# Kernel optimization log

Measured on AMD Instinct MI355X. Metric: run time of the kernel, lower is better.

Reference implementation:

```python
import jax, jax.numpy as jnp
import numpy as np

B, C, H, W = 2, 3, 96, 96
D = 32  # qkv channels

def setup_inputs() -> dict:
    key = jax.random.key(0)
    ks = jax.random.split(key, 9)
    s3 = 1.0 / np.sqrt(3.0)
    sD = 1.0 / np.sqrt(float(D))
    return {
        "image": jax.random.normal(ks[0], (B, C, H, W), dtype=jnp.float32),
        "key_w": jax.random.normal(ks[1], (D, C), dtype=jnp.float32) * s3,
        "key_b": jax.random.normal(ks[2], (D,), dtype=jnp.float32) * 0.01,
        "query_w": jax.random.normal(ks[3], (D, C), dtype=jnp.float32) * s3,
        "query_b": jax.random.normal(ks[4], (D,), dtype=jnp.float32) * 0.01,
        "value_w": jax.random.normal(ks[5], (D, C), dtype=jnp.float32) * s3,
        "value_b": jax.random.normal(ks[6], (D,), dtype=jnp.float32) * 0.01,
        "out_w": jax.random.normal(ks[7], (C, D), dtype=jnp.float32) * sD,
        "out_b": jax.random.normal(ks[8], (C,), dtype=jnp.float32) * 0.01,
    }

def reference(image, key_w, key_b, query_w, query_b, value_w, value_b, out_w, out_b):
    b, c, h, w = image.shape
    n = h * w
    x = image.reshape(b, c, n)  # [B,3,N]
    # 1x1 convs == per-pixel linear maps over channels
    f_x = jnp.einsum('dc,bcn->bdn', key_w, x) + key_b[None, :, None]    # key   [B,D,N]
    g_x = jnp.einsum('dc,bcn->bdn', query_w, x) + query_b[None, :, None]  # query [B,D,N]
    h_x = jnp.einsum('dc,bcn->bdn', value_w, x) + value_b[None, :, None]  # value [B,D,N]
    # s = f_x^T @ g_x : [B,N,N]; softmax over dim=1 (first N axis), as in torch code
    s = jnp.einsum('bdn,bdm->bnm', f_x, g_x)
    beta = jax.nn.softmax(s, axis=1)
    # v = h_x @ beta : [B,D,N]
    v = jnp.einsum('bdn,bnm->bdm', h_x, beta)
    # output 1x1 conv D->3, then clamp
    o = jnp.einsum('cd,bdm->bcm', out_w, v) + out_b[None, :, None]
    o = jnp.clip(o, -1.0, 1.0)
    return o.reshape(b, c, h, w)
```

## Files before the change

kernel.cpp:

```cpp
#include <hip/hip_runtime.h>
#include <hip/hip_fp16.h>

#define BB 2
#define CC 3
#define NN 9216
#define DD 32
#define NSPLIT 4
#define KSPLIT 6
#define KEYS_PER_WAVE (NN / (KSPLIT * NSPLIT))
#define CHUNKS (KEYS_PER_WAVE / 64)
#define NGROUP (BB * NN / 32)
#define L2E 1.44269504f
#define SZH ((size_t)BB * NN * DD)

typedef _Float16 half8 __attribute__((ext_vector_type(8)));
typedef _Float16 half4v __attribute__((ext_vector_type(4)));
typedef __fp16 fp16x2 __attribute__((ext_vector_type(2)));
typedef float float4v __attribute__((ext_vector_type(4)));

#define MFMA_K32(a, b, c) __builtin_amdgcn_mfma_f32_16x16x32_f16((a), (b), (c), 0, 0, 0)

__global__ __launch_bounds__(256) void prep_kernel(
    const float* __restrict__ img,
    const float* __restrict__ kw, const float* __restrict__ kb,
    const float* __restrict__ qw, const float* __restrict__ qb,
    const float* __restrict__ vw, const float* __restrict__ vb,
    const float* __restrict__ ow,
    _Float16* __restrict__ fH, _Float16* __restrict__ fL,
    _Float16* __restrict__ gH, _Float16* __restrict__ gL,
    _Float16* __restrict__ hP)
{
    __shared__ float wsm[256];
    __shared__ float cwb[12];
    int bid = blockIdx.x;
    int t = threadIdx.x;
    if (bid < 288) {
        float v;
        if (t < 96)       v = kw[t];
        else if (t < 192) v = qw[t - 96];
        else if (t < 224) v = kb[t - 192];
        else              v = qb[t - 224];
        wsm[t] = v;
        __syncthreads();

        int id = bid * 256 + t;
        int part = id & 3;
        int n = (id >> 2) % NN;
        int b = (id >> 2) / NN;
        const float* xb = img + (size_t)b * CC * NN + n;
        float x0 = xb[0], x1 = xb[NN], x2 = xb[2 * NN];
        half8 fh, fl, gh, gl;
#pragma unroll
        for (int j = 0; j < 8; j++) {
            int d = part * 8 + j;
            float fv = wsm[d * 3 + 0] * x0 + wsm[d * 3 + 1] * x1 +
                       wsm[d * 3 + 2] * x2 + wsm[192 + d];
            float gv = (wsm[96 + d * 3 + 0] * x0 + wsm[96 + d * 3 + 1] * x1 +
                        wsm[96 + d * 3 + 2] * x2 + wsm[224 + d]) * L2E;
            _Float16 fhi = (_Float16)fv;
            _Float16 ghi = (_Float16)gv;
            fh[j] = fhi; fl[j] = (_Float16)(fv - (float)fhi);
            gh[j] = ghi; gl[j] = (_Float16)(gv - (float)ghi);
        }
        size_t off = ((size_t)b * NN + n) * DD + part * 8;
        *(half8*)(fH + off) = fh;
        *(half8*)(fL + off) = fl;
        *(half8*)(gH + off) = gh;
        *(half8*)(gL + off) = gl;
    } else {
        if (t < 9) {
            int c = t / 3, k = t % 3;
            float s = 0.f;
#pragma unroll
            for (int d = 0; d < DD; d++) s += ow[c * DD + d] * vw[d * 3 + k];
            cwb[t] = s;
        } else if (t < 12) {
            int c = t - 9;
            float s = 0.f;
#pragma unroll
            for (int d = 0; d < DD; d++) s += ow[c * DD + d] * vb[d];
            cwb[9 + c] = s;
        }
        __syncthreads();
        const int N8 = NN / 8;
        int id = (bid - 288) * 256 + t;
        int n8 = id % N8;
        int row = (id / N8) & 3;
        int b = id / (N8 * 4);
        half8 hv = {1, 1, 1, 1, 1, 1, 1, 1};
        if (row < 3) {
            const float* xb = img + (size_t)b * CC * NN + n8 * 8;
            float w0 = cwb[row * 3 + 0], w1 = cwb[row * 3 + 1],
                  w2 = cwb[row * 3 + 2], bv = cwb[9 + row];
#pragma unroll
            for (int j = 0; j < 8; j++)
                hv[j] = (_Float16)(w0 * xb[j] + w1 * xb[NN + j] + w2 * xb[2 * NN + j] + bv);
        }
        *(half8*)(hP + ((size_t)(b * 4 + row)) * NN + n8 * 8) = hv;
    }
}

__device__ __forceinline__ void softmax_store(const float4v* s, float& mrun,
                                              float4v& acc, _Float16* Pw,
                                              int l16, int quad)
{
    float a0 = fmaxf(fmaxf(s[0][0], s[0][1]), s[0][2]);
    float a1 = fmaxf(fmaxf(s[0][3], s[1][0]), s[1][1]);
    float a2 = fmaxf(fmaxf(s[1][2], s[1][3]), s[2][0]);
    float a3 = fmaxf(fmaxf(s[2][1], s[2][2]), s[2][3]);
    float a4 = fmaxf(fmaxf(s[3][0], s[3][1]), s[3][2]);
    float lmax = fmaxf(fmaxf(fmaxf(a0, a1), fmaxf(a2, a3)), fmaxf(a4, s[3][3]));
    if (__any(lmax > mrun + 8.f)) {
        float mx = fmaxf(lmax, __shfl_xor(lmax, 16, 64));
        mx = fmaxf(mx, __shfl_xor(mx, 32, 64));
        float mnew = fmaxf(mrun, mx);
        float alpha = __builtin_amdgcn_exp2f(mrun - mnew);
#pragma unroll
        for (int r = 0; r < 4; r++) acc[r] *= alpha;
        mrun = mnew;
    }
#pragma unroll
    for (int blk = 0; blk < 4; blk++) {
        float p0 = __builtin_amdgcn_exp2f(s[blk][0] - mrun);
        float p1 = __builtin_amdgcn_exp2f(s[blk][1] - mrun);
        float p2 = __builtin_amdgcn_exp2f(s[blk][2] - mrun);
        float p3 = __builtin_amdgcn_exp2f(s[blk][3] - mrun);
        union { fp16x2 h2[2]; half4v h4; } u;
        u.h2[0] = __builtin_amdgcn_cvt_pkrtz(p0, p1);
        u.h2[1] = __builtin_amdgcn_cvt_pkrtz(p2, p3);
        *(half4v*)(Pw + l16 * 72 + blk * 16 + quad * 4) = u.h4;
    }
}

__global__ __launch_bounds__(256)
__attribute__((amdgpu_waves_per_eu(4, 4)))
void attn_partial_kernel(
    const _Float16* __restrict__ ws,
    float* __restrict__ pnum, float* __restrict__ pM)
{
    const _Float16* fH = ws;
    const _Float16* gH = ws + 2 * SZH;
    const _Float16* hP = ws + 4 * SZH;

    const int gb = blockIdx.x;
    const int g  = gb / KSPLIT;
    const int ks = gb % KSPLIT;
    const int b = g / (NN / 32);
    const int m0 = (g % (NN / 32)) * 32;
    const int tid = threadIdx.x;
    const int w = tid >> 6;
    const int lane = tid & 63;
    const int l16 = lane & 15;
    const int quad = lane >> 4;

    union SMem {
        _Float16 P[NSPLIT * 2 * 16 * 72];
        struct { float acc[NSPLIT][4][33]; float mbuf[NSPLIT][32]; } mg;
    };
    __shared__ __align__(16) SMem sm;

    const _Float16* gHb = gH + ((size_t)b * NN + m0 + l16) * DD + quad * 8;
    half8 qh0 = *(const half8*)(gHb);
    half8 ql0 = *(const half8*)(gHb + SZH);
    half8 qh1 = *(const half8*)(gHb + (size_t)16 * DD);
    half8 ql1 = *(const half8*)(gHb + SZH + (size_t)16 * DD);

    float4v acc0 = {0,0,0,0};
    float4v acc1 = {0,0,0,0};
    float mrun0 = -1e30f;
    float mrun1 = -1e30f;

    const int nbase = ks * (NN / KSPLIT) + w * KEYS_PER_WAVE;
    const int vrow = (l16 < 3) ? l16 : 3;
    const _Float16* vp = hP + ((size_t)(b * 4 + vrow)) * NN + nbase + quad * 8;
    const _Float16* kp = fH + ((size_t)b * NN + nbase + l16) * DD + quad * 8;
    const _Float16* lp = kp + SZH;
    _Float16* Pw0 = sm.P + (size_t)(w * 2 + 0) * 16 * 72;
    _Float16* Pw1 = sm.P + (size_t)(w * 2 + 1) * 16 * 72;

    half8 kC[4], lC[4];
#pragma unroll
    for (int blk = 0; blk < 4; blk++) {
        kC[blk] = *(const half8*)(kp + (size_t)(blk * 16) * DD);
        lC[blk] = *(const half8*)(lp + (size_t)(blk * 16) * DD);
    }
    kp += (size_t)64 * DD;
    lp += (size_t)64 * DD;

    for (int c = 0; c < CHUNKS; ++c) {
        float4v s[4];
#pragma unroll
        for (int blk = 0; blk < 4; blk++) {
            float4v z = {0,0,0,0};
            float4v t0 = MFMA_K32(kC[blk], ql0, z);
            t0 = MFMA_K32(lC[blk], qh0, t0);
            s[blk] = MFMA_K32(kC[blk], qh0, t0);
        }
        softmax_store(s, mrun0, acc0, Pw0, l16, quad);

#pragma unroll
        for (int blk = 0; blk < 4; blk++) {
            float4v z = {0,0,0,0};
            float4v t1 = MFMA_K32(kC[blk], ql1, z);
            t1 = MFMA_K32(lC[blk], qh1, t1);
            s[blk] = MFMA_K32(kC[blk], qh1, t1);
            kC[blk] = *(const half8*)(kp + (size_t)(blk * 16) * DD);
            lC[blk] = *(const half8*)(lp + (size_t)(blk * 16) * DD);
        }
        kp += (size_t)64 * DD;
        lp += (size_t)64 * DD;

        half8 vA0 = *(const half8*)(vp);
        half8 vA1 = *(const half8*)(vp + 32);

        softmax_store(s, mrun1, acc1, Pw1, l16, quad);

        {
            half8 pf0 = *(const half8*)(Pw0 + l16 * 72 + quad * 8);
            half8 pf1 = *(const half8*)(Pw0 + l16 * 72 + 32 + quad * 8);
            acc0 = MFMA_K32(vA0, pf0, acc0);
            acc0 = MFMA_K32(vA1, pf1, acc0);
            half8 qf0 = *(const half8*)(Pw1 + l16 * 72 + quad * 8);
            half8 qf1 = *(const half8*)(Pw1 + l16 * 72 + 32 + quad * 8);
            acc1 = MFMA_K32(vA0, qf0, acc1);
            acc1 = MFMA_K32(vA1, qf1, acc1);
        }
        vp += 64;
    }

    __syncthreads();

    if (quad == 0) {
#pragma unroll
        for (int r = 0; r < 4; r++) {
            sm.mg.acc[w][r][l16]      = acc0[r];
            sm.mg.acc[w][r][l16 + 16] = acc1[r];
        }
        sm.mg.mbuf[w][l16]      = mrun0;
        sm.mg.mbuf[w][l16 + 16] = mrun1;
    }
    __syncthreads();

    if (tid < 4 * 32) {
        int c = tid >> 5, m = tid & 31;
        float M = sm.mg.mbuf[0][m];
#pragma unroll
        for (int s2 = 1; s2 < NSPLIT; s2++) M = fmaxf(M, sm.mg.mbuf[s2][m]);
        float v = 0.f;
#pragma unroll
        for (int s2 = 0; s2 < NSPLIT; s2++)
            v += sm.mg.acc[s2][c][m] * __builtin_amdgcn_exp2f(sm.mg.mbuf[s2][m] - M);
        pnum[(size_t)gb * 128 + tid] = v;
        if (c == 0) pM[gb * 32 + m] = M;
    }
}

__global__ __launch_bounds__(128) void merge_kernel(
    const float* __restrict__ pnum, const float* __restrict__ pM,
    const float* __restrict__ ob, float* __restrict__ out)
{
    const int g = blockIdx.x;
    const int b = g / (NN / 32);
    const int m0 = (g % (NN / 32)) * 32;
    const int tid = threadIdx.x;

    if (tid < CC * 32) {
        int c = tid >> 5, m = tid & 31;
        int base = g * KSPLIT;
        float M = pM[base * 32 + m];
#pragma unroll
        for (int k = 1; k < KSPLIT; k++) M = fmaxf(M, pM[(base + k) * 32 + m]);
        float num = 0.f, L = 0.f;
#pragma unroll
        for (int k = 0; k < KSPLIT; k++) {
            float e = __builtin_amdgcn_exp2f(pM[(base + k) * 32 + m] - M);
            num += pnum[(size_t)(base + k) * 128 + c * 32 + m] * e;
            L   += pnum[(size_t)(base + k) * 128 + 96 + m] * e;
        }
        float o = num / L + ob[c];
        o = fminf(1.f, fmaxf(-1.f, o));
        out[((size_t)b * CC + c) * NN + m0 + m] = o;
    }
}

extern "C" void kernel_launch(void* const* d_in, const int* in_sizes, int n_in,
                              void* d_out, int out_size, void* d_ws, size_t ws_size,
                              hipStream_t stream) {
    const float* img = (const float*)d_in[0];
    const float* kw  = (const float*)d_in[1];
    const float* kb  = (const float*)d_in[2];
    const float* qw  = (const float*)d_in[3];
    const float* qb  = (const float*)d_in[4];
    const float* vw  = (const float*)d_in[5];
    const float* vb  = (const float*)d_in[6];
    const float* ow  = (const float*)d_in[7];
    const float* ob  = (const float*)d_in[8];
    float* out = (float*)d_out;

    _Float16* fH = (_Float16*)d_ws;
    _Float16* fL = fH + SZH;
    _Float16* gH = fL + SZH;
    _Float16* gL = gH + SZH;
    _Float16* hP = gL + SZH;
    float* pnum = (float*)(hP + (size_t)BB * 4 * NN);
    float* pM   = pnum + (size_t)NGROUP * KSPLIT * 128;

    prep_kernel<<<324, 256, 0, stream>>>(img, kw, kb, qw, qb, vw, vb, ow,
                                         fH, fL, gH, gL, hP);
    attn_partial_kernel<<<NGROUP * KSPLIT, 256, 0, stream>>>(
        (const _Float16*)d_ws, pnum, pM);
    merge_kernel<<<NGROUP, 128, 0, stream>>>(pnum, pM, ob, out);
}
```

Measured before the change: 133.5 us.

## Remove key split and merge kernel; finalize softmax output inside attention kernel

Drops the KSPLIT split over keys so that each block handles all keys for its 32 queries, and merges the four wave partials in shared memory. The output, including bias and clamp, is then written directly. This removes the merge kernel launch and the global round trip for partial numerators and maxima. In exchange the grid shrinks sixfold and each block's serial loop grows sixfold, which can underfill the GPU.

```diff
diff --git a/kernel.cpp b/kernel.cpp
--- a/kernel.cpp
+++ b/kernel.cpp
@@ -6,8 +6,7 @@
 #define NN 9216
 #define DD 32
 #define NSPLIT 4
-#define KSPLIT 6
-#define KEYS_PER_WAVE (NN / (KSPLIT * NSPLIT))
+#define KEYS_PER_WAVE (NN / NSPLIT)
 #define CHUNKS (KEYS_PER_WAVE / 64)
 #define NGROUP (BB * NN / 32)
 #define L2E 1.44269504f
@@ -134,17 +133,15 @@
 
 __global__ __launch_bounds__(256)
 __attribute__((amdgpu_waves_per_eu(4, 4)))
-void attn_partial_kernel(
+void attn_kernel(
     const _Float16* __restrict__ ws,
-    float* __restrict__ pnum, float* __restrict__ pM)
+    const float* __restrict__ ob, float* __restrict__ out)
 {
     const _Float16* fH = ws;
     const _Float16* gH = ws + 2 * SZH;
     const _Float16* hP = ws + 4 * SZH;
 
-    const int gb = blockIdx.x;
-    const int g  = gb / KSPLIT;
-    const int ks = gb % KSPLIT;
+    const int g  = blockIdx.x;
     const int b = g / (NN / 32);
     const int m0 = (g % (NN / 32)) * 32;
     const int tid = threadIdx.x;
@@ -170,7 +167,7 @@
     float mrun0 = -1e30f;
     float mrun1 = -1e30f;
 
-    const int nbase = ks * (NN / KSPLIT) + w * KEYS_PER_WAVE;
+    const int nbase = w * KEYS_PER_WAVE;
     const int vrow = (l16 < 3) ? l16 : 3;
     const _Float16* vp = hP + ((size_t)(b * 4 + vrow)) * NN + nbase + quad * 8;
     const _Float16* kp = fH + ((size_t)b * NN + nbase + l16) * DD + quad * 8;
@@ -241,41 +238,17 @@
     }
     __syncthreads();
 
-    if (tid < 4 * 32) {
+    if (tid < CC * 32) {
         int c = tid >> 5, m = tid & 31;
         float M = sm.mg.mbuf[0][m];
 #pragma unroll
         for (int s2 = 1; s2 < NSPLIT; s2++) M = fmaxf(M, sm.mg.mbuf[s2][m]);
-        float v = 0.f;
-#pragma unroll
-        for (int s2 = 0; s2 < NSPLIT; s2++)
-            v += sm.mg.acc[s2][c][m] * __builtin_amdgcn_exp2f(sm.mg.mbuf[s2][m] - M);
-        pnum[(size_t)gb * 128 + tid] = v;
-        if (c == 0) pM[gb * 32 + m] = M;
-    }
-}
-
-__global__ __launch_bounds__(128) void merge_kernel(
-    const float* __restrict__ pnum, const float* __restrict__ pM,
-    const float* __restrict__ ob, float* __restrict__ out)
-{
-    const int g = blockIdx.x;
-    const int b = g / (NN / 32);
-    const int m0 = (g % (NN / 32)) * 32;
-    const int tid = threadIdx.x;
-
-    if (tid < CC * 32) {
-        int c = tid >> 5, m = tid & 31;
-        int base = g * KSPLIT;
-        float M = pM[base * 32 + m];
-#pragma unroll
-        for (int k = 1; k < KSPLIT; k++) M = fmaxf(M, pM[(base + k) * 32 + m]);
         float num = 0.f, L = 0.f;
 #pragma unroll
-        for (int k = 0; k < KSPLIT; k++) {
-            float e = __builtin_amdgcn_exp2f(pM[(base + k) * 32 + m] - M);
-            num += pnum[(size_t)(base + k) * 128 + c * 32 + m] * e;
-            L   += pnum[(size_t)(base + k) * 128 + 96 + m] * e;
+        for (int s2 = 0; s2 < NSPLIT; s2++) {
+            float e = __builtin_amdgcn_exp2f(sm.mg.mbuf[s2][m] - M);
+            num += sm.mg.acc[s2][c][m] * e;
+            L   += sm.mg.acc[s2][3][m] * e;
         }
         float o = num / L + ob[c];
         o = fminf(1.f, fmaxf(-1.f, o));
@@ -302,12 +275,8 @@
     _Float16* gH = fL + SZH;
     _Float16* gL = gH + SZH;
     _Float16* hP = gL + SZH;
-    float* pnum = (float*)(hP + (size_t)BB * 4 * NN);
-    float* pM   = pnum + (size_t)NGROUP * KSPLIT * 128;
 
     prep_kernel<<<324, 256, 0, stream>>>(img, kw, kb, qw, qb, vw, vb, ow,
                                          fH, fL, gH, gL, hP);
-    attn_partial_kernel<<<NGROUP * KSPLIT, 256, 0, stream>>>(
-        (const _Float16*)d_ws, pnum, pM);
-    merge_kernel<<<NGROUP, 128, 0, stream>>>(pnum, pM, ob, out);
-}
+    attn_kernel<<<NGROUP, 256, 0, stream>>>((const _Float16*)d_ws, ob, out);
+}
```

After: 138.9 us. 4.1% more time.
